# Kernel optimization log

Hardware: AMD Instinct MI355X
Metric: run time of the kernel (lower is better)

The kernel has to match this reference:

```python
import jax, jax.numpy as jnp
import numpy as np


def _maxpool2x2(x):
    # x: [B, H, W, C] -> [B, H//2, W//2, C], VALID 2x2/2 max pool
    B, H, W, C = x.shape
    return x.reshape(B, H // 2, 2, W // 2, 2, C).max(axis=(2, 4))


def setup_inputs() -> dict:
    key = jax.random.key(0)
    ks = jax.random.split(key, 6)
    B, H, W, C = 16, 64, 64, 512
    x = jax.random.normal(ks[0], (B, H, W, C), dtype=jnp.float32)
    w_theta = jax.random.normal(ks[1], (C, C // 8), dtype=jnp.float32) * 0.02
    w_phi = jax.random.normal(ks[2], (C, C // 8), dtype=jnp.float32) * 0.02
    w_g = jax.random.normal(ks[3], (C, C // 2), dtype=jnp.float32) * 0.02
    w_o = jax.random.normal(ks[4], (C // 2, C), dtype=jnp.float32) * 0.02
    return {
        "x": x,
        "w_theta": w_theta, "b_theta": jnp.zeros((C // 8,), jnp.float32),
        "w_phi": w_phi, "b_phi": jnp.zeros((C // 8,), jnp.float32),
        "w_g": w_g, "b_g": jnp.zeros((C // 2,), jnp.float32),
        "w_o": w_o, "b_o": jnp.zeros((C,), jnp.float32),
        "sigma": jnp.ones((1,), jnp.float32) * 0.1,
    }


def reference(x, w_theta, b_theta, w_phi, b_phi, w_g, b_g, w_o, b_o, sigma):
    B, H, W, C = x.shape
    n_feat = H * W
    # 1x1 convs are channel-mixing GEMMs over pixels
    theta = (jnp.einsum('bhwc,cd->bhwd', x, w_theta) + b_theta).reshape(B, n_feat, C // 8)
    phi = _maxpool2x2(jnp.einsum('bhwc,cd->bhwd', x, w_phi) + b_phi).reshape(B, n_feat // 4, C // 8)
    g = _maxpool2x2(jnp.einsum('bhwc,cd->bhwd', x, w_g) + b_g).reshape(B, n_feat // 4, C // 2)
    # [B, HW, HW/4] attention (no scaling, matching SAGAN/tf source)
    attn = jax.nn.softmax(jnp.einsum('bqd,bkd->bqk', theta, phi), axis=-1)
    attn_g = jnp.einsum('bqk,bkd->bqd', attn, g).reshape(B, H, W, C // 2)
    attn_g = jnp.einsum('bhwd,dc->bhwc', attn_g, w_o) + b_o
    return x + sigma * attn_g
```

## Files before the change

kernel.cpp:

```cpp
#include <hip/hip_runtime.h>
#include <math.h>

#define NB    16
#define NPIX  4096
#define NPOOL 1024
#define CIN   512
#define CD    64
#define CG    256

typedef unsigned short u16;
typedef unsigned int   u32;
typedef __attribute__((ext_vector_type(8)))  u16    u16x8;
typedef __attribute__((ext_vector_type(8)))  __bf16 bf16x8;
typedef __attribute__((ext_vector_type(16))) float  f32x16;

__device__ __forceinline__ u16 f2bf(float x) {
    u32 u = __builtin_bit_cast(u32, x);
    u += 0x7fffu + ((u >> 16) & 1u);
    return (u16)(u >> 16);
}
__device__ __forceinline__ float bf2f(u16 h) {
    u32 u = ((u32)h) << 16;
    return __builtin_bit_cast(float, u);
}
__device__ __forceinline__ f32x16 mfma32(u16x8 a, u16x8 b, f32x16 c) {
    return __builtin_amdgcn_mfma_f32_32x32x16_bf16(
        __builtin_bit_cast(bf16x8, a), __builtin_bit_cast(bf16x8, b), c, 0, 0, 0);
}

__global__ __launch_bounds__(256) void prep_kernel(
    const float* __restrict__ wt, const float* __restrict__ wp,
    const float* __restrict__ wg, const float* __restrict__ wo,
    const float* __restrict__ bt, const float* __restrict__ bp,
    const float* __restrict__ bg,
    u16* __restrict__ WT, u16* __restrict__ WOT, float* __restrict__ biasP)
{
    const int bx = blockIdx.x;
    const int t  = threadIdx.x;

    if (bx == 320) {
        for (int i = t; i < 384; i += 256)
            biasP[i] = (i < 64) ? bt[i] : (i < 128) ? bp[i - 64] : bg[i - 128];
        return;
    }

    const float* src; u16* dst; int N, K, kt, nt;
    if (bx < 32)       { src = wt; dst = WT;             N = 64;  K = 512; kt = bx >> 1;        nt = bx & 1; }
    else if (bx < 64)  { src = wp; dst = WT + 64 * 512;  N = 64;  K = 512; kt = (bx - 32) >> 1; nt = (bx - 32) & 1; }
    else if (bx < 192) { src = wg; dst = WT + 128 * 512; N = 256; K = 512; kt = (bx - 64) >> 3; nt = (bx - 64) & 7; }
    else               { src = wo; dst = WOT;            N = 512; K = 256; kt = (bx - 192) >> 4; nt = (bx - 192) & 15; }

    __shared__ float tile[32][33];
    {
        int r  = t >> 3;
        int c4 = (t & 7) * 4;
        float4 v = *(const float4*)(src + (size_t)(kt * 32 + r) * N + nt * 32 + c4);
        tile[r][c4]     = v.x;
        tile[r][c4 + 1] = v.y;
        tile[r][c4 + 2] = v.z;
        tile[r][c4 + 3] = v.w;
    }
    __syncthreads();
    {
        int n  = t >> 3;
        int k4 = (t & 7) * 4;
        ushort4 wv;
        wv.x = f2bf(tile[k4][n]);
        wv.y = f2bf(tile[k4 + 1][n]);
        wv.z = f2bf(tile[k4 + 2][n]);
        wv.w = f2bf(tile[k4 + 3][n]);
        *(ushort4*)(dst + (size_t)(nt * 32 + n) * K + kt * 32 + k4) = wv;
    }
}

#define AST 40
__global__ __launch_bounds__(256) void proj_gemm_kernel(
    const float* __restrict__ x, const u16* __restrict__ WT,
    const float* __restrict__ biasP,
    u16* __restrict__ theta, u16* __restrict__ phiF, u16* __restrict__ gF)
{
    __shared__ u16 As[128 * AST];
    __shared__ u16 Bs[128 * AST];

    const int t  = threadIdx.x;
    const int w  = t >> 6, l = t & 63, lr = l & 31, lh = l >> 5;
    const int sb = (blockIdx.x & 7) * 192 + (blockIdx.x >> 3);
    const int mt = sb / 3, nt = sb % 3;
    const int m0 = mt * 128, n0 = nt * 128;
    const int mw = (w & 1) * 64, nw = (w >> 1) * 64;

    const int srow = t >> 1;
    const int sks  = (t & 1) * 16;

    f32x16 acc[2][2] = {};

    for (int k0 = 0; k0 < 512; k0 += 32) {
        {
            const float4* ap = (const float4*)(x + (size_t)(m0 + srow) * 512 + k0 + sks);
            float4 v0 = ap[0], v1 = ap[1], v2 = ap[2], v3 = ap[3];
            u16x8 a0, a1;
            a0[0] = f2bf(v0.x); a0[1] = f2bf(v0.y); a0[2] = f2bf(v0.z); a0[3] = f2bf(v0.w);
            a0[4] = f2bf(v1.x); a0[5] = f2bf(v1.y); a0[6] = f2bf(v1.z); a0[7] = f2bf(v1.w);
            a1[0] = f2bf(v2.x); a1[1] = f2bf(v2.y); a1[2] = f2bf(v2.z); a1[3] = f2bf(v2.w);
            a1[4] = f2bf(v3.x); a1[5] = f2bf(v3.y); a1[6] = f2bf(v3.z); a1[7] = f2bf(v3.w);
            *(u16x8*)&As[srow * AST + sks]     = a0;
            *(u16x8*)&As[srow * AST + sks + 8] = a1;
        }
        {
            const u16x8* bp = (const u16x8*)(WT + (size_t)(n0 + srow) * 512 + k0 + sks);
            *(u16x8*)&Bs[srow * AST + sks]     = bp[0];
            *(u16x8*)&Bs[srow * AST + sks + 8] = bp[1];
        }
        __syncthreads();
#pragma unroll
        for (int ki = 0; ki < 2; ++ki) {
            u16x8 af0 = *(const u16x8*)&As[(mw + lr)      * AST + ki * 16 + lh * 8];
            u16x8 af1 = *(const u16x8*)&As[(mw + 32 + lr) * AST + ki * 16 + lh * 8];
            u16x8 bf0 = *(const u16x8*)&Bs[(nw + lr)      * AST + ki * 16 + lh * 8];
            u16x8 bf1 = *(const u16x8*)&Bs[(nw + 32 + lr) * AST + ki * 16 + lh * 8];
            acc[0][0] = mfma32(af0, bf0, acc[0][0]);
            acc[0][1] = mfma32(af0, bf1, acc[0][1]);
            acc[1][0] = mfma32(af1, bf0, acc[1][0]);
            acc[1][1] = mfma32(af1, bf1, acc[1][1]);
        }
        __syncthreads();
    }

#pragma unroll
    for (int mi = 0; mi < 2; ++mi) {
#pragma unroll
        for (int ni = 0; ni < 2; ++ni) {
            const int nb = n0 + nw + ni * 32;
            const int n  = nb + lr;
            const float bv = biasP[n];
            u16* dst; int ld, col;
            if (nb < 64)        { dst = theta; ld = 64;  col = n; }
            else if (nb < 128)  { dst = phiF;  ld = 64;  col = n - 64; }
            else                { dst = gF;    ld = 256; col = n - 128; }
#pragma unroll
            for (int r = 0; r < 16; ++r) {
                int row = m0 + mw + mi * 32 + (r & 3) + 8 * (r >> 2) + 4 * lh;
                dst[(size_t)row * ld + col] = f2bf(acc[mi][ni][r] + bv);
            }
        }
    }
}

__global__ __launch_bounds__(256) void pool_kernel(
    const u16* __restrict__ phiF, const u16* __restrict__ gF,
    u16* __restrict__ phi, u16* __restrict__ gt)
{
    const int t  = threadIdx.x;
    const int b  = blockIdx.x >> 5;
    const int ph = blockIdx.x & 31;

    {
        const int pw = t >> 3, dq = (t & 7) * 8;
        const u16* base = phiF + ((size_t)(b * NPIX + 2 * ph * 64 + 2 * pw)) * 64 + dq;
        u16x8 v00 = *(const u16x8*)(base);
        u16x8 v01 = *(const u16x8*)(base + 64);
        u16x8 v10 = *(const u16x8*)(base + 64 * 64);
        u16x8 v11 = *(const u16x8*)(base + 64 * 64 + 64);
        u16x8 m;
#pragma unroll
        for (int j = 0; j < 8; ++j) {
            float mf = fmaxf(fmaxf(bf2f(v00[j]), bf2f(v01[j])),
                             fmaxf(bf2f(v10[j]), bf2f(v11[j])));
            m[j] = f2bf(mf);
        }
        *(u16x8*)(phi + ((size_t)(b * NPOOL + ph * 32 + pw)) * 64 + dq) = m;
    }
    {
        const u16* gb = gF + ((size_t)(b * NPIX + 2 * ph * 64)) * 256 + t;
        u16 buf[32];
#pragma unroll
        for (int kp = 0; kp < 32; ++kp) {
            float m = fmaxf(
                fmaxf(bf2f(gb[(size_t)(2 * kp) * 256]),      bf2f(gb[(size_t)(2 * kp + 1) * 256])),
                fmaxf(bf2f(gb[(size_t)(64 + 2 * kp) * 256]), bf2f(gb[(size_t)(64 + 2 * kp + 1) * 256])));
            buf[kp] = f2bf(m);
        }
        u16* go = gt + ((size_t)(b * CG + t)) * NPOOL + ph * 32;
#pragma unroll
        for (int j = 0; j < 4; ++j)
            *(u16x8*)(go + j * 8) = *(const u16x8*)&buf[j * 8];
    }
}

#define SLD 1032
__global__ __launch_bounds__(512) void attn_mfma_kernel(
    const u16* __restrict__ theta, const u16* __restrict__ phi,
    const u16* __restrict__ gt, u16* __restrict__ attn_g)
{
    __shared__ u16   S[64 * SLD];
    __shared__ float rinv[64];

    const int t  = threadIdx.x;
    const int w  = t >> 6;
    const int l  = t & 63;
    const int lr = l & 31;
    const int lh = l >> 5;
    const int sb = (blockIdx.x & 7) * 128 + (blockIdx.x >> 3);
    const int b  = sb >> 6;
    const int q0 = (sb & 63) * 64;

    const u16* thb0 = theta + ((size_t)(b * NPIX + q0 + lr)) * CD + lh * 8;
    const u16* thb1 = thb0 + (size_t)32 * CD;
    u16x8 af0[4], af1[4];
#pragma unroll
    for (int ki = 0; ki < 4; ++ki) {
        af0[ki] = *(const u16x8*)(thb0 + ki * 16);
        af1[ki] = *(const u16x8*)(thb1 + ki * 16);
    }

    const u16* phb = phi + (size_t)b * NPOOL * CD;
#pragma unroll 2
    for (int nt = 0; nt < 4; ++nt) {
        int k0 = w * 128 + nt * 32;
        const u16* pb = phb + (size_t)(k0 + lr) * CD + lh * 8;
        u16x8 pf0 = *(const u16x8*)(pb);
        u16x8 pf1 = *(const u16x8*)(pb + 16);
        u16x8 pf2 = *(const u16x8*)(pb + 32);
        u16x8 pf3 = *(const u16x8*)(pb + 48);
        f32x16 acc0 = {}, acc1 = {};
        acc0 = mfma32(af0[0], pf0, acc0);  acc1 = mfma32(af1[0], pf0, acc1);
        acc0 = mfma32(af0[1], pf1, acc0);  acc1 = mfma32(af1[1], pf1, acc1);
        acc0 = mfma32(af0[2], pf2, acc0);  acc1 = mfma32(af1[2], pf2, acc1);
        acc0 = mfma32(af0[3], pf3, acc0);  acc1 = mfma32(af1[3], pf3, acc1);
#pragma unroll
        for (int r = 0; r < 16; ++r) {
            int row = (r & 3) + 8 * (r >> 2) + 4 * lh;
            S[row * SLD + k0 + lr]        = f2bf(acc0[r]);
            S[(32 + row) * SLD + k0 + lr] = f2bf(acc1[r]);
        }
    }
    __syncthreads();

    {
        const int row = t >> 3, cg = t & 7;
        u16* srow = S + row * SLD;
        float mx = -1e30f;
#pragma unroll
        for (int i = 0; i < 16; ++i) {
            u16x8 v = *(const u16x8*)(srow + cg * 8 + 64 * i);
#pragma unroll
            for (int j = 0; j < 8; ++j) mx = fmaxf(mx, bf2f(v[j]));
        }
        mx = fmaxf(mx, __shfl_xor(mx, 1));
        mx = fmaxf(mx, __shfl_xor(mx, 2));
        mx = fmaxf(mx, __shfl_xor(mx, 4));
        float sum = 0.f;
#pragma unroll
        for (int i = 0; i < 16; ++i) {
            u16* p = srow + cg * 8 + 64 * i;
            u16x8 v = *(const u16x8*)p;
            u16x8 e;
#pragma unroll
            for (int j = 0; j < 8; ++j) {
                float ev = __expf(bf2f(v[j]) - mx);
                sum += ev;
                e[j] = f2bf(ev);
            }
            *(u16x8*)p = e;
        }
        sum += __shfl_xor(sum, 1);
        sum += __shfl_xor(sum, 2);
        sum += __shfl_xor(sum, 4);
        if (cg == 0) rinv[row] = 1.0f / sum;
    }
    __syncthreads();

    const u16* gp  = gt + ((size_t)(b * CG + w * 32 + lr)) * NPOOL + lh * 8;
    const u16* ar0 = S + lr * SLD + lh * 8;
    const u16* ar1 = S + (32 + lr) * SLD + lh * 8;
    f32x16 o0a = {}, o0b = {}, o1a = {}, o1b = {};
#pragma unroll 4
    for (int k0 = 0; k0 < NPOOL; k0 += 32) {
        u16x8 b0  = *(const u16x8*)(gp + k0);
        u16x8 b1  = *(const u16x8*)(gp + k0 + 16);
        u16x8 a00 = *(const u16x8*)(ar0 + k0);
        u16x8 a01 = *(const u16x8*)(ar0 + k0 + 16);
        u16x8 a10 = *(const u16x8*)(ar1 + k0);
        u16x8 a11 = *(const u16x8*)(ar1 + k0 + 16);
        o0a = mfma32(a00, b0, o0a);
        o0b = mfma32(a01, b1, o0b);
        o1a = mfma32(a10, b0, o1a);
        o1b = mfma32(a11, b1, o1b);
    }

    u16* obp = attn_g + ((size_t)(b * NPIX + q0)) * CG;
#pragma unroll
    for (int r = 0; r < 16; ++r) {
        int qrow = (r & 3) + 8 * (r >> 2) + 4 * lh;
        float inv0 = rinv[qrow];
        float inv1 = rinv[32 + qrow];
        obp[(size_t)qrow * CG + w * 32 + lr]        = f2bf((o0a[r] + o0b[r]) * inv0);
        obp[(size_t)(32 + qrow) * CG + w * 32 + lr] = f2bf((o1a[r] + o1b[r]) * inv1);
    }
}

__global__ __launch_bounds__(256) void out_gemm_kernel(
    const u16* __restrict__ attn_gB, const u16* __restrict__ WOT,
    const float* __restrict__ x, const float* __restrict__ bo,
    const float* __restrict__ sigma, float* __restrict__ out)
{
    __shared__ u16 As[128 * AST];
    __shared__ u16 Bs[128 * AST];

    const int t  = threadIdx.x;
    const int w  = t >> 6, l = t & 63, lr = l & 31, lh = l >> 5;
    const int sb = (blockIdx.x & 7) * 256 + (blockIdx.x >> 3);
    const int mt = sb >> 2, nt = sb & 3;
    const int m0 = mt * 128, n0 = nt * 128;
    const int mw = (w & 1) * 64, nw = (w >> 1) * 64;

    const int srow = t >> 1;
    const int sks  = (t & 1) * 16;

    f32x16 acc[2][2] = {};

    for (int k0 = 0; k0 < 256; k0 += 32) {
        {
            const u16x8* ap = (const u16x8*)(attn_gB + (size_t)(m0 + srow) * 256 + k0 + sks);
            *(u16x8*)&As[srow * AST + sks]     = ap[0];
            *(u16x8*)&As[srow * AST + sks + 8] = ap[1];
        }
        {
            const u16x8* bp = (const u16x8*)(WOT + (size_t)(n0 + srow) * 256 + k0 + sks);
            *(u16x8*)&Bs[srow * AST + sks]     = bp[0];
            *(u16x8*)&Bs[srow * AST + sks + 8] = bp[1];
        }
        __syncthreads();
#pragma unroll
        for (int ki = 0; ki < 2; ++ki) {
            u16x8 af0 = *(const u16x8*)&As[(mw + lr)      * AST + ki * 16 + lh * 8];
            u16x8 af1 = *(const u16x8*)&As[(mw + 32 + lr) * AST + ki * 16 + lh * 8];
            u16x8 bf0 = *(const u16x8*)&Bs[(nw + lr)      * AST + ki * 16 + lh * 8];
            u16x8 bf1 = *(const u16x8*)&Bs[(nw + 32 + lr) * AST + ki * 16 + lh * 8];
            acc[0][0] = mfma32(af0, bf0, acc[0][0]);
            acc[0][1] = mfma32(af0, bf1, acc[0][1]);
            acc[1][0] = mfma32(af1, bf0, acc[1][0]);
            acc[1][1] = mfma32(af1, bf1, acc[1][1]);
        }
        __syncthreads();
    }

    const float s = sigma[0];
#pragma unroll
    for (int mi = 0; mi < 2; ++mi) {
#pragma unroll
        for (int ni = 0; ni < 2; ++ni) {
            const int n  = n0 + nw + ni * 32 + lr;
            const float bv = bo[n];
#pragma unroll
            for (int r = 0; r < 16; ++r) {
                int row = m0 + mw + mi * 32 + (r & 3) + 8 * (r >> 2) + 4 * lh;
                size_t idx = (size_t)row * 512 + n;
                out[idx] = x[idx] + s * (acc[mi][ni][r] + bv);
            }
        }
    }
}

extern "C" void kernel_launch(void* const* d_in, const int* in_sizes, int n_in,
                              void* d_out, int out_size, void* d_ws, size_t ws_size,
                              hipStream_t stream)
{
    const float* x     = (const float*)d_in[0];
    const float* wt    = (const float*)d_in[1];
    const float* bt    = (const float*)d_in[2];
    const float* wp    = (const float*)d_in[3];
    const float* bp    = (const float*)d_in[4];
    const float* wg    = (const float*)d_in[5];
    const float* bg    = (const float*)d_in[6];
    const float* wo    = (const float*)d_in[7];
    const float* bo    = (const float*)d_in[8];
    const float* sigma = (const float*)d_in[9];
    float* out = (float*)d_out;

    char* ws = (char*)d_ws;
    u16*   theta   = (u16*)(ws);
    u16*   phi     = (u16*)(ws + ((size_t)8  << 20));
    u16*   phiF    = (u16*)(ws + ((size_t)10 << 20));
    u16*   gF      = (u16*)(ws + ((size_t)18 << 20));
    u16*   attn_gB = (u16*)(ws + ((size_t)10 << 20));
    u16*   gt      = (u16*)(ws + ((size_t)50 << 20));
    u16*   WT      = (u16*)(ws + ((size_t)58 << 20));
    u16*   WOT     = (u16*)(ws + ((size_t)58 << 20) + (384 << 10));
    float* biasP   = (float*)(ws + ((size_t)58 << 20) + (640 << 10));

    prep_kernel<<<321, 256, 0, stream>>>(wt, wp, wg, wo, bt, bp, bg, WT, WOT, biasP);
    proj_gemm_kernel<<<512 * 3, 256, 0, stream>>>(x, WT, biasP, theta, phiF, gF);
    pool_kernel<<<NB * 32, 256, 0, stream>>>(phiF, gF, phi, gt);
    attn_mfma_kernel<<<NB * NPIX / 64, 512, 0, stream>>>(theta, phi, gt, attn_gB);
    out_gemm_kernel<<<512 * 4, 256, 0, stream>>>(attn_gB, WOT, x, bo, sigma, out);
}
```

Baseline: 450.4 us.

## Double attention block to 1024 threads and split PV work per wave

The attention kernel now launches 1024 threads per block instead of 512. Each wave computes half as many QK^T key tiles, softmax uses 16 threads per row, and in the PV stage each wave owns one 32-query half and one 32-channel slice rather than both halves. s_setprio is also raised around the MFMA pair. The aim is more waves in flight to hide LDS and global latency within the roughly 130KB LDS per block, which allows one block per CU. The cost is that B fragments of gt are now loaded by two waves each, and the larger block adds barrier overhead.

```diff
diff --git a/kernel.cpp b/kernel.cpp
--- a/kernel.cpp
+++ b/kernel.cpp
@@ -188,7 +188,7 @@
 }
 
 #define SLD 1032
-__global__ __launch_bounds__(512) void attn_mfma_kernel(
+__global__ __launch_bounds__(1024) void attn_mfma_kernel(
     const u16* __restrict__ theta, const u16* __restrict__ phi,
     const u16* __restrict__ gt, u16* __restrict__ attn_g)
 {
@@ -214,9 +214,9 @@
     }
 
     const u16* phb = phi + (size_t)b * NPOOL * CD;
-#pragma unroll 2
-    for (int nt = 0; nt < 4; ++nt) {
-        int k0 = w * 128 + nt * 32;
+#pragma unroll
+    for (int nt = 0; nt < 2; ++nt) {
+        int k0 = w * 64 + nt * 32;
         const u16* pb = phb + (size_t)(k0 + lr) * CD + lh * 8;
         u16x8 pf0 = *(const u16x8*)(pb);
         u16x8 pf1 = *(const u16x8*)(pb + 16);
@@ -237,22 +237,23 @@
     __syncthreads();
 
     {
-        const int row = t >> 3, cg = t & 7;
+        const int row = t >> 4, cg = t & 15;
         u16* srow = S + row * SLD;
         float mx = -1e30f;
 #pragma unroll
-        for (int i = 0; i < 16; ++i) {
-            u16x8 v = *(const u16x8*)(srow + cg * 8 + 64 * i);
+        for (int i = 0; i < 8; ++i) {
+            u16x8 v = *(const u16x8*)(srow + cg * 8 + 128 * i);
 #pragma unroll
             for (int j = 0; j < 8; ++j) mx = fmaxf(mx, bf2f(v[j]));
         }
         mx = fmaxf(mx, __shfl_xor(mx, 1));
         mx = fmaxf(mx, __shfl_xor(mx, 2));
         mx = fmaxf(mx, __shfl_xor(mx, 4));
+        mx = fmaxf(mx, __shfl_xor(mx, 8));
         float sum = 0.f;
 #pragma unroll
-        for (int i = 0; i < 16; ++i) {
-            u16* p = srow + cg * 8 + 64 * i;
+        for (int i = 0; i < 8; ++i) {
+            u16* p = srow + cg * 8 + 128 * i;
             u16x8 v = *(const u16x8*)p;
             u16x8 e;
 #pragma unroll
@@ -266,36 +267,33 @@
         sum += __shfl_xor(sum, 1);
         sum += __shfl_xor(sum, 2);
         sum += __shfl_xor(sum, 4);
+        sum += __shfl_xor(sum, 8);
         if (cg == 0) rinv[row] = 1.0f / sum;
     }
     __syncthreads();
 
-    const u16* gp  = gt + ((size_t)(b * CG + w * 32 + lr)) * NPOOL + lh * 8;
-    const u16* ar0 = S + lr * SLD + lh * 8;
-    const u16* ar1 = S + (32 + lr) * SLD + lh * 8;
-    f32x16 o0a = {}, o0b = {}, o1a = {}, o1b = {};
-#pragma unroll 4
+    const int qt = w & 1, cg3 = w >> 1;
+    const u16* gp  = gt + ((size_t)(b * CG + cg3 * 32 + lr)) * NPOOL + lh * 8;
+    const u16* ar  = S + (qt * 32 + lr) * SLD + lh * 8;
+    f32x16 oa = {}, ob2 = {};
+#pragma unroll 8
     for (int k0 = 0; k0 < NPOOL; k0 += 32) {
-        u16x8 b0  = *(const u16x8*)(gp + k0);
-        u16x8 b1  = *(const u16x8*)(gp + k0 + 16);
-        u16x8 a00 = *(const u16x8*)(ar0 + k0);
-        u16x8 a01 = *(const u16x8*)(ar0 + k0 + 16);
-        u16x8 a10 = *(const u16x8*)(ar1 + k0);
-        u16x8 a11 = *(const u16x8*)(ar1 + k0 + 16);
-        o0a = mfma32(a00, b0, o0a);
-        o0b = mfma32(a01, b1, o0b);
-        o1a = mfma32(a10, b0, o1a);
-        o1b = mfma32(a11, b1, o1b);
-    }
-
-    u16* obp = attn_g + ((size_t)(b * NPIX + q0)) * CG;
+        u16x8 a0 = *(const u16x8*)(ar + k0);
+        u16x8 a1 = *(const u16x8*)(ar + k0 + 16);
+        u16x8 b0 = *(const u16x8*)(gp + k0);
+        u16x8 b1 = *(const u16x8*)(gp + k0 + 16);
+        __builtin_amdgcn_s_setprio(1);
+        oa  = mfma32(a0, b0, oa);
+        ob2 = mfma32(a1, b1, ob2);
+        __builtin_amdgcn_s_setprio(0);
+    }
+
+    u16* obp = attn_g + ((size_t)(b * NPIX + q0 + qt * 32)) * CG;
 #pragma unroll
     for (int r = 0; r < 16; ++r) {
         int qrow = (r & 3) + 8 * (r >> 2) + 4 * lh;
-        float inv0 = rinv[qrow];
-        float inv1 = rinv[32 + qrow];
-        obp[(size_t)qrow * CG + w * 32 + lr]        = f2bf((o0a[r] + o0b[r]) * inv0);
-        obp[(size_t)(32 + qrow) * CG + w * 32 + lr] = f2bf((o1a[r] + o1b[r]) * inv1);
+        float inv = rinv[qt * 32 + qrow];
+        obp[(size_t)qrow * CG + cg3 * 32 + lr] = f2bf((oa[r] + ob2[r]) * inv);
     }
 }
 
@@ -392,6 +390,6 @@
     prep_kernel<<<321, 256, 0, stream>>>(wt, wp, wg, wo, bt, bp, bg, WT, WOT, biasP);
     proj_gemm_kernel<<<512 * 3, 256, 0, stream>>>(x, WT, biasP, theta, phiF, gF);
     pool_kernel<<<NB * 32, 256, 0, stream>>>(phiF, gF, phi, gt);
-    attn_mfma_kernel<<<NB * NPIX / 64, 512, 0, stream>>>(theta, phi, gt, attn_gB);
+    attn_mfma_kernel<<<NB * NPIX / 64, 1024, 0, stream>>>(theta, phi, gt, attn_gB);
     out_gemm_kernel<<<512 * 4, 256, 0, stream>>>(attn_gB, WOT, x, bo, sigma, out);
 }
```

After: 501.2 us. +11.3%, slower.

## Store pooled phi and g in MFMA-fragment-native layout for coalesced attention loads

Applied to the files above, without the earlier changes.

The pool kernel now writes phi and transposed g in a layout where each MFMA lane's 8-element fragment sits contiguously per 32-key block. Each wave's 64 lanes then read one contiguous 1 KB chunk instead of strided rows. The aim is fewer memory transactions and better cache-line use in the attention kernel's global B-operand loads. In exchange, the pool kernel's store pattern and the indexing in both kernels become more complex.

```diff
diff --git a/kernel.cpp b/kernel.cpp
--- a/kernel.cpp
+++ b/kernel.cpp
@@ -148,7 +148,7 @@
 
 __global__ __launch_bounds__(256) void pool_kernel(
     const u16* __restrict__ phiF, const u16* __restrict__ gF,
-    u16* __restrict__ phi, u16* __restrict__ gt)
+    u16* __restrict__ phif, u16* __restrict__ gtf)
 {
     const int t  = threadIdx.x;
     const int b  = blockIdx.x >> 5;
@@ -168,7 +168,8 @@
                              fmaxf(bf2f(v10[j]), bf2f(v11[j])));
             m[j] = f2bf(mf);
         }
-        *(u16x8*)(phi + ((size_t)(b * NPOOL + ph * 32 + pw)) * 64 + dq) = m;
+        const int ki = dq >> 4, lhw = (dq >> 3) & 1;
+        *(u16x8*)(phif + (((size_t)(b * 32 + ph) * 4 + ki) * 64 + (pw * 2 + lhw)) * 8) = m;
     }
     {
         const u16* gb = gF + ((size_t)(b * NPIX + 2 * ph * 64)) * 256 + t;
@@ -180,17 +181,21 @@
                 fmaxf(bf2f(gb[(size_t)(64 + 2 * kp) * 256]), bf2f(gb[(size_t)(64 + 2 * kp + 1) * 256])));
             buf[kp] = f2bf(m);
         }
-        u16* go = gt + ((size_t)(b * CG + t)) * NPOOL + ph * 32;
-#pragma unroll
-        for (int j = 0; j < 4; ++j)
-            *(u16x8*)(go + j * 8) = *(const u16x8*)&buf[j * 8];
+        const int db = t >> 5, lr = t & 31;
+        u16* go = gtf + (((size_t)(b * 32 + ph) * 8 + db) * 2) * 512;
+#pragma unroll
+        for (int h = 0; h < 2; ++h)
+#pragma unroll
+            for (int lhw = 0; lhw < 2; ++lhw)
+                *(u16x8*)(go + h * 512 + (lr * 2 + lhw) * 8) =
+                    *(const u16x8*)&buf[h * 16 + lhw * 8];
     }
 }
 
 #define SLD 1032
 __global__ __launch_bounds__(512) void attn_mfma_kernel(
-    const u16* __restrict__ theta, const u16* __restrict__ phi,
-    const u16* __restrict__ gt, u16* __restrict__ attn_g)
+    const u16* __restrict__ theta, const u16* __restrict__ phif,
+    const u16* __restrict__ gtf, u16* __restrict__ attn_g)
 {
     __shared__ u16   S[64 * SLD];
     __shared__ float rinv[64];
@@ -200,6 +205,7 @@
     const int l  = t & 63;
     const int lr = l & 31;
     const int lh = l >> 5;
+    const int lslot = (lr * 2 + lh) * 8;
     const int sb = (blockIdx.x & 7) * 128 + (blockIdx.x >> 3);
     const int b  = sb >> 6;
     const int q0 = (sb & 63) * 64;
@@ -213,15 +219,15 @@
         af1[ki] = *(const u16x8*)(thb1 + ki * 16);
     }
 
-    const u16* phb = phi + (size_t)b * NPOOL * CD;
 #pragma unroll 2
     for (int nt = 0; nt < 4; ++nt) {
-        int k0 = w * 128 + nt * 32;
-        const u16* pb = phb + (size_t)(k0 + lr) * CD + lh * 8;
+        const int kb = w * 4 + nt;
+        const int k0 = kb * 32;
+        const u16* pb = phif + ((size_t)(b * 32 + kb) * 4) * 512 + lslot;
         u16x8 pf0 = *(const u16x8*)(pb);
-        u16x8 pf1 = *(const u16x8*)(pb + 16);
-        u16x8 pf2 = *(const u16x8*)(pb + 32);
-        u16x8 pf3 = *(const u16x8*)(pb + 48);
+        u16x8 pf1 = *(const u16x8*)(pb + 512);
+        u16x8 pf2 = *(const u16x8*)(pb + 1024);
+        u16x8 pf3 = *(const u16x8*)(pb + 1536);
         f32x16 acc0 = {}, acc1 = {};
         acc0 = mfma32(af0[0], pf0, acc0);  acc1 = mfma32(af1[0], pf0, acc1);
         acc0 = mfma32(af0[1], pf1, acc0);  acc1 = mfma32(af1[1], pf1, acc1);
@@ -270,18 +276,20 @@
     }
     __syncthreads();
 
-    const u16* gp  = gt + ((size_t)(b * CG + w * 32 + lr)) * NPOOL + lh * 8;
-    const u16* ar0 = S + lr * SLD + lh * 8;
-    const u16* ar1 = S + (32 + lr) * SLD + lh * 8;
+    const u16* gfb = gtf + ((size_t)(b * 32) * 16 + (size_t)w * 2) * 512 + lslot;
+    const u16* ar0 = S + lr * SLD;
+    const u16* ar1 = S + (32 + lr) * SLD;
     f32x16 o0a = {}, o0b = {}, o1a = {}, o1b = {};
 #pragma unroll 4
-    for (int k0 = 0; k0 < NPOOL; k0 += 32) {
-        u16x8 b0  = *(const u16x8*)(gp + k0);
-        u16x8 b1  = *(const u16x8*)(gp + k0 + 16);
-        u16x8 a00 = *(const u16x8*)(ar0 + k0);
-        u16x8 a01 = *(const u16x8*)(ar0 + k0 + 16);
-        u16x8 a10 = *(const u16x8*)(ar1 + k0);
-        u16x8 a11 = *(const u16x8*)(ar1 + k0 + 16);
+    for (int kb = 0; kb < 32; ++kb) {
+        const u16* gpk = gfb + (size_t)kb * (16 * 512);
+        u16x8 b0  = *(const u16x8*)(gpk);
+        u16x8 b1  = *(const u16x8*)(gpk + 512);
+        const int k0 = kb * 32;
+        u16x8 a00 = *(const u16x8*)(ar0 + k0 + lh * 8);
+        u16x8 a01 = *(const u16x8*)(ar0 + k0 + 16 + lh * 8);
+        u16x8 a10 = *(const u16x8*)(ar1 + k0 + lh * 8);
+        u16x8 a11 = *(const u16x8*)(ar1 + k0 + 16 + lh * 8);
         o0a = mfma32(a00, b0, o0a);
         o0b = mfma32(a01, b1, o0b);
         o1a = mfma32(a10, b0, o1a);
@@ -380,18 +388,18 @@
 
     char* ws = (char*)d_ws;
     u16*   theta   = (u16*)(ws);
-    u16*   phi     = (u16*)(ws + ((size_t)8  << 20));
+    u16*   phif    = (u16*)(ws + ((size_t)8  << 20));
     u16*   phiF    = (u16*)(ws + ((size_t)10 << 20));
     u16*   gF      = (u16*)(ws + ((size_t)18 << 20));
     u16*   attn_gB = (u16*)(ws + ((size_t)10 << 20));
-    u16*   gt      = (u16*)(ws + ((size_t)50 << 20));
+    u16*   gtf     = (u16*)(ws + ((size_t)50 << 20));
     u16*   WT      = (u16*)(ws + ((size_t)58 << 20));
     u16*   WOT     = (u16*)(ws + ((size_t)58 << 20) + (384 << 10));
     float* biasP   = (float*)(ws + ((size_t)58 << 20) + (640 << 10));
 
     prep_kernel<<<321, 256, 0, stream>>>(wt, wp, wg, wo, bt, bp, bg, WT, WOT, biasP);
     proj_gemm_kernel<<<512 * 3, 256, 0, stream>>>(x, WT, biasP, theta, phiF, gF);
-    pool_kernel<<<NB * 32, 256, 0, stream>>>(phiF, gF, phi, gt);
-    attn_mfma_kernel<<<NB * NPIX / 64, 512, 0, stream>>>(theta, phi, gt, attn_gB);
+    pool_kernel<<<NB * 32, 256, 0, stream>>>(phiF, gF, phif, gtf);
+    attn_mfma_kernel<<<NB * NPIX / 64, 512, 0, stream>>>(theta, phif, gtf, attn_gB);
     out_gemm_kernel<<<512 * 4, 256, 0, stream>>>(attn_gB, WOT, x, bo, sigma, out);
 }
```

Measured after the change: 417.5 us. 1.08x faster.
